# Optimization experiments

Hardware: AMD Instinct MI355X
Metric: run time of the kernel (lower is better)

The kernel has to match this reference:

```python
import jax, jax.numpy as jnp
import numpy as np

OUT_F, IN_F = 4096, 4096
BLOCK = 64  # bitsandbytes NF4 block size

# NF4 code table (bitsandbytes): 16 quantile levels of a standard normal, scaled to [-1, 1]
NF4_CODE = jnp.array([
    -1.0, -0.6961928009986877, -0.5250730514526367, -0.39491748809814453,
    -0.28444138169288635, -0.18477343022823334, -0.09105003625154495, 0.0,
    0.07958029955625534, 0.16093020141124725, 0.24611230194568634, 0.33791524171829224,
    0.44070982933044434, 0.5626170039176941, 0.7229568362236023, 1.0,
], dtype=jnp.float32)


def dequantize_nf4(packed, absmax):
    # packed: [OUT_F*IN_F//2] int values in [0,256); two 4-bit indices per byte (high nibble first)
    hi = (packed >> 4) & 0xF
    lo = packed & 0xF
    idx = jnp.stack([hi, lo], axis=-1).reshape(-1)           # [OUT_F*IN_F]
    vals = NF4_CODE[idx]                                      # lookup
    vals = vals.reshape(-1, BLOCK) * absmax[:, None]          # per-block scale
    return vals.reshape(OUT_F, IN_F)


def setup_inputs() -> dict:
    key = jax.random.key(0)
    k1, k2, k3, k4 = jax.random.split(key, 4)
    x = jax.random.normal(k1, (4, 2048, IN_F), dtype=jnp.float32)
    packed_weight = jax.random.randint(k2, (OUT_F * IN_F // 2,), 0, 256, dtype=jnp.int32)
    absmax = jax.random.uniform(k3, (OUT_F * IN_F // BLOCK,), dtype=jnp.float32)
    bias = jax.random.normal(k4, (OUT_F,), dtype=jnp.float32)
    return {"x": x, "packed_weight": packed_weight, "absmax": absmax, "bias": bias}


def reference(x, packed_weight, absmax, bias):
    weight = dequantize_nf4(packed_weight, absmax)            # [OUT_F, IN_F]
    # F.linear: x @ W^T + b
    return jnp.einsum('bsi,oi->bso', x, weight) + bias
```

## Files before the change

### kernel.cpp

```cpp
#include <hip/hip_runtime.h>
#include <hip/hip_bf16.h>
#include <stdint.h>

#define IN_F   4096
#define OUT_F  4096
#define MROWS  8192
#define NT     64

typedef __bf16 bf16x8 __attribute__((ext_vector_type(8)));
typedef float  f32x4  __attribute__((ext_vector_type(4)));
typedef unsigned short ushort8v __attribute__((ext_vector_type(8)));

__device__ __constant__ float NF4_TAB[16] = {
    -1.0f, -0.6961928009986877f, -0.5250730514526367f, -0.39491748809814453f,
    -0.28444138169288635f, -0.18477343022823334f, -0.09105003625154495f, 0.0f,
    0.07958029955625534f, 0.16093020141124725f, 0.24611230194568634f, 0.33791524171829224f,
    0.44070982933044434f, 0.5626170039176941f, 0.7229568362236023f, 1.0f,
};

__device__ __forceinline__ unsigned short f2bf_rne(float f) {
    unsigned u = __builtin_bit_cast(unsigned, f);
    return (unsigned short)((u + 0x7FFFu + ((u >> 16) & 1u)) >> 16);
}

__global__ __launch_bounds__(256) void prep_kernel(
        const float* __restrict__ x, const int* __restrict__ packed,
        const float* __restrict__ absmax,
        unsigned short* __restrict__ Wb, unsigned short* __restrict__ Xb) {
    __shared__ float tab[16];
    if (threadIdx.x < 16) tab[threadIdx.x] = NF4_TAB[threadIdx.x];
    __syncthreads();

    const int bid = blockIdx.x;
    if (bid < 512) {
        const int ngroups = OUT_F * IN_F / 8;
        const int stride = 512 * 256;
        for (int g = bid * 256 + threadIdx.x; g < ngroups; g += stride) {
            int4 pv = reinterpret_cast<const int4*>(packed)[g];
            float am = absmax[g >> 3];
            ushort8v o;
            o[0] = f2bf_rne(tab[(pv.x >> 4) & 0xF] * am);
            o[1] = f2bf_rne(tab[ pv.x       & 0xF] * am);
            o[2] = f2bf_rne(tab[(pv.y >> 4) & 0xF] * am);
            o[3] = f2bf_rne(tab[ pv.y       & 0xF] * am);
            o[4] = f2bf_rne(tab[(pv.z >> 4) & 0xF] * am);
            o[5] = f2bf_rne(tab[ pv.z       & 0xF] * am);
            o[6] = f2bf_rne(tab[(pv.w >> 4) & 0xF] * am);
            o[7] = f2bf_rne(tab[ pv.w       & 0xF] * am);
            *reinterpret_cast<ushort8v*>(&Wb[(size_t)g * 8]) = o;
        }
    } else {
        const int ngroups = MROWS * IN_F / 8;
        const int stride = 1536 * 256;
        for (int g = (bid - 512) * 256 + threadIdx.x; g < ngroups; g += stride) {
            float4 v0 = reinterpret_cast<const float4*>(x)[2 * g];
            float4 v1 = reinterpret_cast<const float4*>(x)[2 * g + 1];
            ushort8v o;
            o[0] = f2bf_rne(v0.x); o[1] = f2bf_rne(v0.y);
            o[2] = f2bf_rne(v0.z); o[3] = f2bf_rne(v0.w);
            o[4] = f2bf_rne(v1.x); o[5] = f2bf_rne(v1.y);
            o[6] = f2bf_rne(v1.z); o[7] = f2bf_rne(v1.w);
            *reinterpret_cast<ushort8v*>(&Xb[(size_t)g * 8]) = o;
        }
    }
}

#define GLOAD16(gp, lp)                                                        \
    __builtin_amdgcn_global_load_lds(                                          \
        (const __attribute__((address_space(1))) void*)(gp),                   \
        (__attribute__((address_space(3))) void*)(lp), 16, 0, 0)

#define BARF()  asm volatile("s_barrier" ::: "memory")
#define VMW(n)  asm volatile("s_waitcnt vmcnt(" #n ")" ::: "memory")

__global__ __launch_bounds__(512) void gemm256_kernel(
        const unsigned short* __restrict__ A,
        const unsigned short* __restrict__ B,
        const float* __restrict__ bias,
        float* __restrict__ C) {
    __shared__ __align__(16) unsigned short lds[65536];

    const int tid  = threadIdx.x;
    const int lane = tid & 63;
    const int wave = tid >> 6;
    const int wr   = wave >> 2;
    const int wcn  = wave & 3;
    const int lr   = lane & 15;
    const int lg   = lane >> 4;

    const int bid = blockIdx.x;
    const int wg  = (bid & 7) * 64 + (bid >> 3);
    const int bm  = (wg >> 4) << 8;
    const int bn  = (wg & 15) << 8;

    int srow[2], skel[2];
#pragma unroll
    for (int r = 0; r < 2; ++r) {
        int c = tid + r * 512;
        int L = c * 16;
        int sw = L ^ (((L >> 7) & 7) << 4);
        srow[r] = sw >> 6;
        skel[r] = (sw & 63) >> 1;
    }
    const unsigned short* pA0 = A + (size_t)(bm + srow[0]) * IN_F + skel[0];
    const unsigned short* pA1 = A + (size_t)(bm + srow[1]) * IN_F + skel[1];
    const unsigned short* pB0 = B + (size_t)(bn + srow[0]) * IN_F + skel[0];
    const unsigned short* pB1 = B + (size_t)(bn + srow[1]) * IN_F + skel[1];
    const int d0 = tid * 8, d1 = tid * 8 + 4096;

#define STAGE_A(t, kh) do {                                                    \
        int _b = ((t) & 1) * 32768 + (kh) * 8192;                              \
        int _k = (t) * 64 + (kh) * 32;                                         \
        GLOAD16(pA0 + _k, &lds[_b + d0]);                                      \
        GLOAD16(pA1 + _k, &lds[_b + d1]); } while (0)
#define STAGE_B(t, kh) do {                                                    \
        int _b = ((t) & 1) * 32768 + 16384 + (kh) * 8192;                      \
        int _k = (t) * 64 + (kh) * 32;                                         \
        GLOAD16(pB0 + _k, &lds[_b + d0]);                                      \
        GLOAD16(pB1 + _k, &lds[_b + d1]); } while (0)

    const int laneoff = ((lr * 64 + lg * 16) ^ (((lr >> 1) & 7) << 4)) >> 1;
    const int arow = wr * 128;
    const int brow = wcn * 64;

    f32x4  acc[8][4] = {};
    bf16x8 af0[4], af1[4], bfv[4];

#define LOADB(b, kh) do {                                                      \
        int _base = (b) * 32768 + 16384 + (kh) * 8192 + brow * 32 + laneoff;   \
        bfv[0] = *reinterpret_cast<const bf16x8*>(&lds[_base]);                \
        bfv[1] = *reinterpret_cast<const bf16x8*>(&lds[_base + 512]);          \
        bfv[2] = *reinterpret_cast<const bf16x8*>(&lds[_base + 1024]);         \
        bfv[3] = *reinterpret_cast<const bf16x8*>(&lds[_base + 1536]); } while (0)
#define LOADA(b, kh, mq, dst) do {                                             \
        int _base = (b) * 32768 + (kh) * 8192 + (arow + (mq) * 64) * 32 + laneoff; \
        dst[0] = *reinterpret_cast<const bf16x8*>(&lds[_base]);                \
        dst[1] = *reinterpret_cast<const bf16x8*>(&lds[_base + 512]);          \
        dst[2] = *reinterpret_cast<const bf16x8*>(&lds[_base + 1024]);         \
        dst[3] = *reinterpret_cast<const bf16x8*>(&lds[_base + 1536]); } while (0)

#define MFMA32() do {                                                          \
        __builtin_amdgcn_s_setprio(1);                                         \
        _Pragma("unroll")                                                      \
        for (int mi = 0; mi < 4; ++mi)                                         \
            _Pragma("unroll")                                                  \
            for (int ni = 0; ni < 4; ++ni)                                     \
                acc[mi][ni] = __builtin_amdgcn_mfma_f32_16x16x32_bf16(         \
                    af0[mi], bfv[ni], acc[mi][ni], 0, 0, 0);                   \
        _Pragma("unroll")                                                      \
        for (int mi = 0; mi < 4; ++mi)                                         \
            _Pragma("unroll")                                                  \
            for (int ni = 0; ni < 4; ++ni)                                     \
                acc[4 + mi][ni] = __builtin_amdgcn_mfma_f32_16x16x32_bf16(     \
                    af1[mi], bfv[ni], acc[4 + mi][ni], 0, 0, 0);               \
        __builtin_amdgcn_s_setprio(0); } while (0)

#define PHASE(b, kh, S1, S2, V) do {                                           \
        LOADB(b, kh); LOADA(b, kh, 0, af0); LOADA(b, kh, 1, af1);              \
        S1; S2; MFMA32(); V; BARF(); } while (0)

    STAGE_A(0, 0); STAGE_B(0, 0); STAGE_A(0, 1);
    STAGE_B(0, 1); STAGE_A(1, 0); STAGE_B(1, 0);
    VMW(6);
    BARF();

#pragma unroll 2
    for (int t = 0; t < NT - 2; ++t) {
        const int b = t & 1;
        PHASE(b, 0, STAGE_A(t + 1, 1), STAGE_B(t + 1, 1), VMW(6));
        PHASE(b, 1, STAGE_A(t + 2, 0), STAGE_B(t + 2, 0), VMW(6));
    }
    PHASE(0, 0, STAGE_A(63, 1), STAGE_B(63, 1), VMW(6));
    PHASE(0, 1, , , VMW(4));
    PHASE(1, 0, , , VMW(0));
    PHASE(1, 1, , , );

#pragma unroll
    for (int a = 0; a < 8; ++a) {
        const int row0 = bm + wr * 128 + (a >> 2) * 64 + (a & 3) * 16 + lg * 4;
#pragma unroll
        for (int ni = 0; ni < 4; ++ni) {
            const int col = bn + wcn * 64 + ni * 16 + lr;
            const float bs = bias[col];
            float* cp = C + (size_t)row0 * OUT_F + col;
#pragma unroll
            for (int j = 0; j < 4; ++j)
                cp[(size_t)j * OUT_F] = acc[a][ni][j] + bs;
        }
    }
}

extern "C" void kernel_launch(void* const* d_in, const int* in_sizes, int n_in,
                              void* d_out, int out_size, void* d_ws, size_t ws_size,
                              hipStream_t stream) {
    const float* x      = (const float*)d_in[0];
    const int*   packed = (const int*)d_in[1];
    const float* absmax = (const float*)d_in[2];
    const float* bias   = (const float*)d_in[3];
    float* out = (float*)d_out;

    unsigned short* Wb = (unsigned short*)d_ws;
    unsigned short* Xb = Wb + (size_t)OUT_F * IN_F;

    prep_kernel<<<2048, 256, 0, stream>>>(x, packed, absmax, Wb, Xb);
    gemm256_kernel<<<512, 512, 0, stream>>>(Xb, Wb, bias, out);
}
```

Before: 484.6 us.

## Switch GEMM inner loop from 16x16x32 to 32x32x16 bf16 MFMA tiles

Replaces the 16x16x32 MFMA micro-tile arrangement with 32x32x16 MFMAs. Each wave still covers its 128x64 output tile, now as 4x2 32x32 accumulators instead of 8x4 16x16 ones. LDS fragment addressing and the epilogue store mapping are rewritten for the 32x32 output layout. The larger MFMA shape needs fewer LDS fragment loads per FLOP and fewer instructions. The trade-off is a different LDS read pattern, which could introduce bank conflicts under the existing swizzle, and a more strided output write pattern.

```diff
diff --git a/kernel.cpp b/kernel.cpp
--- a/kernel.cpp
+++ b/kernel.cpp
@@ -8,7 +8,7 @@
 #define NT     64
 
 typedef __bf16 bf16x8 __attribute__((ext_vector_type(8)));
-typedef float  f32x4  __attribute__((ext_vector_type(4)));
+typedef float  f32x16 __attribute__((ext_vector_type(16)));
 typedef unsigned short ushort8v __attribute__((ext_vector_type(8)));
 
 __device__ __constant__ float NF4_TAB[16] = {
@@ -85,8 +85,8 @@
     const int wave = tid >> 6;
     const int wr   = wave >> 2;
     const int wcn  = wave & 3;
-    const int lr   = lane & 15;
-    const int lg   = lane >> 4;
+    const int ll   = lane & 31;
+    const int hi   = lane >> 5;
 
     const int bid = blockIdx.x;
     const int wg  = (bid & 7) * 64 + (bid >> 3);
@@ -119,45 +119,44 @@
         GLOAD16(pB0 + _k, &lds[_b + d0]);                                      \
         GLOAD16(pB1 + _k, &lds[_b + d1]); } while (0)
 
-    const int laneoff = ((lr * 64 + lg * 16) ^ (((lr >> 1) & 7) << 4)) >> 1;
-    const int arow = wr * 128;
-    const int brow = wcn * 64;
-
-    f32x4  acc[8][4] = {};
-    bf16x8 af0[4], af1[4], bfv[4];
-
-#define LOADB(b, kh) do {                                                      \
-        int _base = (b) * 32768 + 16384 + (kh) * 8192 + brow * 32 + laneoff;   \
-        bfv[0] = *reinterpret_cast<const bf16x8*>(&lds[_base]);                \
-        bfv[1] = *reinterpret_cast<const bf16x8*>(&lds[_base + 512]);          \
-        bfv[2] = *reinterpret_cast<const bf16x8*>(&lds[_base + 1024]);         \
-        bfv[3] = *reinterpret_cast<const bf16x8*>(&lds[_base + 1536]); } while (0)
-#define LOADA(b, kh, mq, dst) do {                                             \
-        int _base = (b) * 32768 + (kh) * 8192 + (arow + (mq) * 64) * 32 + laneoff; \
-        dst[0] = *reinterpret_cast<const bf16x8*>(&lds[_base]);                \
-        dst[1] = *reinterpret_cast<const bf16x8*>(&lds[_base + 512]);          \
-        dst[2] = *reinterpret_cast<const bf16x8*>(&lds[_base + 1024]);         \
-        dst[3] = *reinterpret_cast<const bf16x8*>(&lds[_base + 1536]); } while (0)
-
-#define MFMA32() do {                                                          \
+    const int lb   = ll * 64 + hi * 16;
+    const int amt  = ((ll >> 1) & 7) << 4;
+    const int lo0  = ((lb)      ^ amt) >> 1;
+    const int lo1  = ((lb + 32) ^ amt) >> 1;
+    const int arow = wr * 4096;
+    const int brow = wcn * 2048;
+
+    f32x16 acc[4][2] = {};
+    bf16x8 af[4][2], bfv[2][2];
+
+#define LOADAB(b, kh) do {                                                     \
+        int _ab = (b) * 32768 + (kh) * 8192 + arow;                            \
+        int _bb = (b) * 32768 + 16384 + (kh) * 8192 + brow;                    \
+        _Pragma("unroll")                                                      \
+        for (int mi = 0; mi < 4; ++mi) {                                       \
+            af[mi][0] = *reinterpret_cast<const bf16x8*>(&lds[_ab + mi*1024 + lo0]); \
+            af[mi][1] = *reinterpret_cast<const bf16x8*>(&lds[_ab + mi*1024 + lo1]); \
+        }                                                                      \
+        _Pragma("unroll")                                                      \
+        for (int ni = 0; ni < 2; ++ni) {                                       \
+            bfv[ni][0] = *reinterpret_cast<const bf16x8*>(&lds[_bb + ni*1024 + lo0]); \
+            bfv[ni][1] = *reinterpret_cast<const bf16x8*>(&lds[_bb + ni*1024 + lo1]); \
+        } } while (0)
+
+#define MFMA16() do {                                                          \
         __builtin_amdgcn_s_setprio(1);                                         \
         _Pragma("unroll")                                                      \
-        for (int mi = 0; mi < 4; ++mi)                                         \
+        for (int s = 0; s < 2; ++s)                                            \
             _Pragma("unroll")                                                  \
-            for (int ni = 0; ni < 4; ++ni)                                     \
-                acc[mi][ni] = __builtin_amdgcn_mfma_f32_16x16x32_bf16(         \
-                    af0[mi], bfv[ni], acc[mi][ni], 0, 0, 0);                   \
-        _Pragma("unroll")                                                      \
-        for (int mi = 0; mi < 4; ++mi)                                         \
-            _Pragma("unroll")                                                  \
-            for (int ni = 0; ni < 4; ++ni)                                     \
-                acc[4 + mi][ni] = __builtin_amdgcn_mfma_f32_16x16x32_bf16(     \
-                    af1[mi], bfv[ni], acc[4 + mi][ni], 0, 0, 0);               \
+            for (int mi = 0; mi < 4; ++mi)                                     \
+                _Pragma("unroll")                                              \
+                for (int ni = 0; ni < 2; ++ni)                                 \
+                    acc[mi][ni] = __builtin_amdgcn_mfma_f32_32x32x16_bf16(     \
+                        af[mi][s], bfv[ni][s], acc[mi][ni], 0, 0, 0);          \
         __builtin_amdgcn_s_setprio(0); } while (0)
 
 #define PHASE(b, kh, S1, S2, V) do {                                           \
-        LOADB(b, kh); LOADA(b, kh, 0, af0); LOADA(b, kh, 1, af1);              \
-        S1; S2; MFMA32(); V; BARF(); } while (0)
+        LOADAB(b, kh); S1; S2; MFMA16(); V; BARF(); } while (0)
 
     STAGE_A(0, 0); STAGE_B(0, 0); STAGE_A(0, 1);
     STAGE_B(0, 1); STAGE_A(1, 0); STAGE_B(1, 0);
@@ -176,16 +175,17 @@
     PHASE(1, 1, , , );
 
 #pragma unroll
-    for (int a = 0; a < 8; ++a) {
-        const int row0 = bm + wr * 128 + (a >> 2) * 64 + (a & 3) * 16 + lg * 4;
-#pragma unroll
-        for (int ni = 0; ni < 4; ++ni) {
-            const int col = bn + wcn * 64 + ni * 16 + lr;
+    for (int mi = 0; mi < 4; ++mi) {
+#pragma unroll
+        for (int ni = 0; ni < 2; ++ni) {
+            const int col = bn + wcn * 64 + ni * 32 + ll;
             const float bs = bias[col];
-            float* cp = C + (size_t)row0 * OUT_F + col;
-#pragma unroll
-            for (int j = 0; j < 4; ++j)
-                cp[(size_t)j * OUT_F] = acc[a][ni][j] + bs;
+            const int rbase = bm + wr * 128 + mi * 32 + 4 * hi;
+#pragma unroll
+            for (int j = 0; j < 16; ++j) {
+                const int row = rbase + (j & 3) + 8 * (j >> 2);
+                C[(size_t)row * OUT_F + col] = acc[mi][ni][j] + bs;
+            }
         }
     }
 }
```

Measured after the change: 512.7 us. 5.8% more time.
